# Performance work log

Hardware: AMD Instinct MI355X
Metric: run time of the kernel (lower is better)

Reference implementation:

```python
import jax, jax.numpy as jnp
import numpy as np

L, H, E, FF, B, S = 2, 8, 512, 2048, 8, 1024


def _layernorm(x, g, b, eps=1e-5):
    mu = jnp.mean(x, axis=-1, keepdims=True)
    var = jnp.mean(jnp.square(x - mu), axis=-1, keepdims=True)
    return (x - mu) * jax.lax.rsqrt(var + eps) * g + b


def setup_inputs() -> dict:
    key = jax.random.key(0)
    ks = jax.random.split(key, 16)
    sc = 1.0 / np.sqrt(E)
    d = {
        "x": jax.random.normal(ks[0], (B, S, E), jnp.float32),
        # per-layer, per-head disentangled projections: Linear(E,E) -> weight [out,in]
        "Wq": jax.random.normal(ks[1], (L, H, E, E), jnp.float32) * sc,
        "bq": jnp.zeros((L, H, E), jnp.float32),
        "Wk": jax.random.normal(ks[2], (L, H, E, E), jnp.float32) * sc,
        "bk": jnp.zeros((L, H, E), jnp.float32),
        "Wv": jax.random.normal(ks[3], (L, H, E, E), jnp.float32) * sc,
        "bv": jnp.zeros((L, H, E), jnp.float32),
        "Wo": jax.random.normal(ks[4], (L, H, E, E), jnp.float32) * sc,
        "bo": jnp.zeros((L, H, E), jnp.float32),
        "head_alphas": jax.random.uniform(ks[5], (H,), jnp.float32, 0.5, 1.5),
        "ln1_g": jnp.ones((L, E), jnp.float32),
        "ln1_b": jnp.zeros((L, E), jnp.float32),
        "W1": jax.random.normal(ks[6], (L, FF, E), jnp.float32) * sc,
        "b1": jnp.zeros((L, FF), jnp.float32),
        "W2": jax.random.normal(ks[7], (L, E, FF), jnp.float32) * (1.0 / np.sqrt(FF)),
        "b2": jnp.zeros((L, E), jnp.float32),
        "ln2_g": jnp.ones((L, E), jnp.float32),
        "ln2_b": jnp.zeros((L, E), jnp.float32),
    }
    return d


def reference(x, Wq, bq, Wk, bk, Wv, bv, Wo, bo, head_alphas,
              ln1_g, ln1_b, W1, b1, W2, b2, ln2_g, ln2_b):
    seq = x.shape[1]
    # causal additive mask, as generate_square_subsequent_mask
    causal = jnp.where(jnp.tril(jnp.ones((seq, seq), bool)), 0.0, -jnp.inf).astype(x.dtype)
    scale = jnp.sqrt(jnp.asarray(E, x.dtype))  # head_dim == embed_dim (disentangled)
    ha = head_alphas[None, :, None, None]
    for i in range(L):
        # disentangled per-head projections, batched over heads: [B,H,S,E]
        rq = jnp.einsum('bse,hoe->bhso', x, Wq[i]) + bq[i][None, :, None, :]
        rk = jnp.einsum('bse,hoe->bhso', x, Wk[i]) + bk[i][None, :, None, :]
        rv = jnp.einsum('bse,hoe->bhso', x, Wv[i]) + bv[i][None, :, None, :]
        scores = jnp.einsum('bhqd,bhkd->bhqk', rq, rk) / scale + causal
        attn = jax.nn.softmax(scores, axis=-1)
        ao = jnp.einsum('bhqk,bhkd->bhqd', attn, rv) * ha
        # per-head out_proj then sum over heads
        attn_out = jnp.einsum('bhsd,hod->bso', ao, Wo[i]) + jnp.sum(bo[i], axis=0)
        x = _layernorm(x + attn_out, ln1_g[i], ln1_b[i])
        h = jax.nn.relu(jnp.einsum('bse,fe->bsf', x, W1[i]) + b1[i])
        ff = jnp.einsum('bsf,ef->bse', h, W2[i]) + b2[i]
        x = _layernorm(x + ff, ln2_g[i], ln2_b[i])
    return x
```

## Files before the change

kernel.cpp:

```cpp
#include <hip/hip_runtime.h>
#include <hip/hip_bf16.h>
#include <stdint.h>

#define LL 2
#define HH 8
#define EE 512
#define FFD 2048
#define BB 8
#define SS 1024
#define CB 4
#define NCH (BB / CB)
#define PAIRS (CB * HH)

typedef unsigned short u16;
typedef __attribute__((ext_vector_type(8))) short bf16x8;
typedef __attribute__((ext_vector_type(4))) float f32x4;
typedef __attribute__((ext_vector_type(4))) int int4v;
typedef __attribute__((ext_vector_type(2))) int int2v;

__device__ __forceinline__ u16 f2bf(float f){
  union { float f; unsigned u; } c; c.f = f;
  unsigned r = (c.u + 0x7FFFu + ((c.u >> 16) & 1u)) >> 16;
  return (u16)r;
}

struct GP {
  const u16* A; const u16* B;
  const float* bias; const float* resid;
  void* out;
  long AsMHi, AsMLo, AsH;
  long BsNHi, BsNLo, BsH;
  long Abatch, Bbatch, Obatch, BiasB;
  long OsMHi, OsMLo, OsNHi, OsNLo;
  int M, N, K, causal, Kpart, cgrid;
  float scale;
};

__device__ __forceinline__ int xcd_swz(int bid, int nwg){
  if (nwg < 16) return bid;
  const int q = nwg >> 3, r = nwg & 7;
  const int xcd = bid & 7, loc = bid >> 3;
  return (xcd < r ? xcd * (q + 1) : r * (q + 1) + (xcd - r) * q) + loc;
}

template<int EP>
__global__ __launch_bounds__(256, 3) void k_gemm(GP p){
  const int tilesN = p.N >> 7;
  const int tilesM = p.M >> 7;
  const int bid = xcd_swz(blockIdx.x, gridDim.x);
  int mI, nI;
  if (p.cgrid){ nI = bid / tilesM; mI = bid % tilesM; }
  else        { mI = bid / tilesN; nI = bid % tilesN; }
  const int m0 = mI << 7;
  const int n0 = nI << 7;
  if (EP == 0 && p.causal && n0 > m0) return;
  const long bb = blockIdx.y;
  const u16* __restrict__ Ag = p.A + bb * p.Abatch;
  const u16* __restrict__ Bg = p.B + bb * p.Bbatch;

  __shared__ __align__(16) u16 As[128 * 64];
  __shared__ __align__(16) u16 Bs[128 * 64];
  char* AsB = (char*)As;
  char* BsB = (char*)Bs;

  const int t = threadIdx.x;
  const int lane = t & 63;
  const int wv = t >> 6;
  const int wr = (wv >> 1) << 6;
  const int wc = (wv & 1) << 6;

  long aoff[4], boff[4];
  #pragma unroll
  for (int j = 0; j < 4; ++j){
    const int r = ((wv << 2) + j) * 8 + (lane >> 3);
    const int kx = ((lane & 7) << 3) ^ ((r & 7) << 3);
    const int gm = m0 + r;
    aoff[j] = (long)(gm >> 10) * p.AsMHi + (long)(gm & 1023) * p.AsMLo + kx;
    const int gn = n0 + r;
    boff[j] = (long)(gn >> 9) * p.BsNHi + (long)(gn & 511) * p.BsNLo + kx;
  }

  int kBeg = 0;
  int Klim = p.K;
  if (EP == 2 && p.causal) { int kl = m0 + 128; Klim = kl < p.K ? kl : p.K; }
  if (EP == 5) { kBeg = (int)bb * p.Kpart; Klim = kBeg + p.Kpart; }

  f32x4 acc[4][4];
  #pragma unroll
  for (int a = 0; a < 4; ++a)
    #pragma unroll
    for (int b = 0; b < 4; ++b)
      acc[a][b] = (f32x4){0.f, 0.f, 0.f, 0.f};

  for (int k0 = kBeg; k0 < Klim; k0 += 64){
    const long ka = (long)(k0 >> 9) * p.AsH + (k0 & 511);
    const long kb = (long)(k0 >> 9) * p.BsH + (k0 & 511);
    __syncthreads();
    #pragma unroll
    for (int j = 0; j < 4; ++j){
      const int ldsOff = (((wv << 2) + j) << 9);
      __builtin_amdgcn_global_load_lds(
          (const __attribute__((address_space(1))) void*)(Ag + aoff[j] + ka),
          (__attribute__((address_space(3))) void*)(As + ldsOff), 16, 0, 0);
      __builtin_amdgcn_global_load_lds(
          (const __attribute__((address_space(1))) void*)(Bg + boff[j] + kb),
          (__attribute__((address_space(3))) void*)(Bs + ldsOff), 16, 0, 0);
    }
    __syncthreads();
    #pragma unroll
    for (int kk = 0; kk < 2; ++kk){
      bf16x8 af[4], bv[4];
      #pragma unroll
      for (int mi = 0; mi < 4; ++mi){
        int row = wr + (mi << 4) + (lane & 15);
        int bc = ((kk << 6) + ((lane >> 4) << 4)) ^ ((row & 7) << 4);
        af[mi] = *reinterpret_cast<const bf16x8*>(AsB + row * 128 + bc);
      }
      #pragma unroll
      for (int ni = 0; ni < 4; ++ni){
        int row = wc + (ni << 4) + (lane & 15);
        int bc = ((kk << 6) + ((lane >> 4) << 4)) ^ ((row & 7) << 4);
        bv[ni] = *reinterpret_cast<const bf16x8*>(BsB + row * 128 + bc);
      }
      #pragma unroll
      for (int mi = 0; mi < 4; ++mi)
        #pragma unroll
        for (int ni = 0; ni < 4; ++ni)
          acc[mi][ni] = __builtin_amdgcn_mfma_f32_16x16x32_bf16(af[mi], bv[ni], acc[mi][ni], 0, 0, 0);
    }
  }

  const int cm = (lane >> 4) << 2;
  const int cn = lane & 15;
  float biasv[4];
  if (EP == 1 || EP == 4){
    #pragma unroll
    for (int ni = 0; ni < 4; ++ni)
      biasv[ni] = p.bias[bb * p.BiasB + n0 + wc + (ni << 4) + cn];
  }
  #pragma unroll
  for (int mi = 0; mi < 4; ++mi){
    #pragma unroll
    for (int i = 0; i < 4; ++i){
      const int m = m0 + wr + (mi << 4) + cm + i;
      const long ob = bb * p.Obatch + (long)(m >> 10) * p.OsMHi + (long)(m & 1023) * p.OsMLo;
      #pragma unroll
      for (int ni = 0; ni < 4; ++ni){
        const int n = n0 + wc + (ni << 4) + cn;
        const long oa = ob + (long)(n >> 9) * p.OsNHi + (long)(n & 511) * p.OsNLo;
        float v = acc[mi][ni][i];
        if (EP == 0) ((u16*)p.out)[oa] = f2bf(v * p.scale);
        else if (EP == 1) ((u16*)p.out)[oa] = f2bf(v + biasv[ni]);
        else if (EP == 2) ((u16*)p.out)[oa] = f2bf(v);
        else if (EP == 5) ((float*)p.out)[oa] = v;
        else { float r = v + biasv[ni]; ((u16*)p.out)[oa] = f2bf(r > 0.f ? r : 0.f); }
      }
    }
  }
}

__global__ __launch_bounds__(128) void k_redln(const float* __restrict__ part,
                                               const float* __restrict__ bias,
                                               const float* __restrict__ resid,
                                               const float* __restrict__ g,
                                               const float* __restrict__ b,
                                               float* __restrict__ fdst,
                                               u16* __restrict__ bdst,
                                               long rowBase, long mn){
  const long lrow = blockIdx.x;
  const long row = rowBase + lrow;
  const int t = threadIdx.x;
  const int col = t << 2;
  const long poff = lrow * EE + col;
  const long off = row * EE + col;
  f32x4 s = *reinterpret_cast<const f32x4*>(part + poff);
  #pragma unroll
  for (int q = 1; q < 4; ++q){
    f32x4 v = *reinterpret_cast<const f32x4*>(part + q * mn + poff);
    s.x += v.x; s.y += v.y; s.z += v.z; s.w += v.w;
  }
  f32x4 bv = *reinterpret_cast<const f32x4*>(bias + col);
  f32x4 rv = *reinterpret_cast<const f32x4*>(resid + off);
  s.x += bv.x + rv.x; s.y += bv.y + rv.y; s.z += bv.z + rv.z; s.w += bv.w + rv.w;

  float ps = s.x + s.y + s.z + s.w;
  #pragma unroll
  for (int o = 32; o; o >>= 1) ps += __shfl_xor(ps, o);
  __shared__ float red[2], red2[2];
  if ((t & 63) == 0) red[t >> 6] = ps;
  __syncthreads();
  const float mean = (red[0] + red[1]) * (1.0f / EE);
  f32x4 d = { s.x - mean, s.y - mean, s.z - mean, s.w - mean };
  float pv = d.x * d.x + d.y * d.y + d.z * d.z + d.w * d.w;
  #pragma unroll
  for (int o = 32; o; o >>= 1) pv += __shfl_xor(pv, o);
  if ((t & 63) == 0) red2[t >> 6] = pv;
  __syncthreads();
  const float var = (red2[0] + red2[1]) * (1.0f / EE);
  const float rstd = rsqrtf(var + 1e-5f);
  f32x4 gv = *reinterpret_cast<const f32x4*>(g + col);
  f32x4 bb = *reinterpret_cast<const f32x4*>(b + col);
  f32x4 o4 = { d.x * rstd * gv.x + bb.x, d.y * rstd * gv.y + bb.y,
               d.z * rstd * gv.z + bb.z, d.w * rstd * gv.w + bb.w };
  *reinterpret_cast<f32x4*>(fdst + off) = o4;
  union { u16 us[4]; int2v v; } u;
  u.us[0] = f2bf(o4.x); u.us[1] = f2bf(o4.y);
  u.us[2] = f2bf(o4.z); u.us[3] = f2bf(o4.w);
  *reinterpret_cast<int2v*>(bdst + off) = u.v;
}

struct SetupP {
  const float *x, *bq, *bk, *bv, *bo;
  float *xf, *catb, *bos;
  u16 *xb;
};
#define SETUP_TA 524288u
#define SETUP_TC 25600u
__global__ __launch_bounds__(256) void k_setup(SetupP sp){
  const unsigned t = blockIdx.x * 256 + threadIdx.x;
  if (t < SETUP_TA){
    const int i = (int)t << 3;
    f32x4 a = *reinterpret_cast<const f32x4*>(sp.x + i);
    f32x4 b = *reinterpret_cast<const f32x4*>(sp.x + i + 4);
    *reinterpret_cast<f32x4*>(sp.xf + i) = a;
    *reinterpret_cast<f32x4*>(sp.xf + i + 4) = b;
    union { u16 us[8]; int4v v; } u;
    #pragma unroll
    for (int j = 0; j < 4; ++j){ u.us[j] = f2bf(a[j]); u.us[4 + j] = f2bf(b[j]); }
    *reinterpret_cast<int4v*>(sp.xb + i) = u.v;
  } else {
    const int j = (int)(t - SETUP_TA);
    if (j >= 2 * 12800) return;
    const int L = j / 12800;
    const int r = j - L * 12800;
    const int lw = L * HH * EE;
    float* catL = sp.catb + (size_t)L * 3 * HH * EE;
    if (r < 4096) catL[r] = sp.bq[lw + r];
    else if (r < 8192) catL[r] = sp.bk[lw + r - 4096];
    else if (r < 12288) catL[r] = sp.bv[lw + r - 8192];
    else {
      const int o = r - 12288;
      float s = 0.f;
      #pragma unroll
      for (int h = 0; h < HH; ++h) s += sp.bo[lw + h * EE + o];
      sp.bos[L * EE + o] = s;
    }
  }
}

struct WcvtP { const float *Wq, *Wk, *Wv, *Wo, *W1, *W2; u16* wdst; };
#define WCVT_T 1310720u
__global__ __launch_bounds__(256) void k_wcvt(WcvtP wp){
  const unsigned t = blockIdx.x * 256 + threadIdx.x;
  if (t >= WCVT_T) return;
  const size_t j = ((size_t)t) << 3;
  const size_t R = (size_t)2097152;
  const size_t F = (size_t)1048576;
  const float* src; size_t loc;
  if      (j < R)       { src = wp.Wq; loc = j; }
  else if (j < 2*R)     { src = wp.Wk; loc = j - R; }
  else if (j < 3*R)     { src = wp.Wv; loc = j - 2*R; }
  else if (j < 4*R)     { src = wp.Wo; loc = j - 3*R; }
  else if (j < 4*R + F) { src = wp.W1; loc = j - 4*R; }
  else                  { src = wp.W2; loc = j - 4*R - F; }
  f32x4 a = *reinterpret_cast<const f32x4*>(src + loc);
  f32x4 b = *reinterpret_cast<const f32x4*>(src + loc + 4);
  union { u16 us[8]; int4v v; } u;
  #pragma unroll
  for (int q = 0; q < 4; ++q){ u.us[q] = f2bf(a[q]); u.us[4 + q] = f2bf(b[q]); }
  *reinterpret_cast<int4v*>(wp.wdst + j) = u.v;
}

#define SM_BLOCKS (PAIRS * SS / 4)
__global__ __launch_bounds__(256) void k_smt(u16* __restrict__ sp,
                                             const float* __restrict__ alphas,
                                             const u16* __restrict__ v,
                                             u16* __restrict__ vt){
  if (blockIdx.x < SM_BLOCKS){
    const int wv = threadIdx.x >> 6;
    const long row = (long)blockIdx.x * 4 + wv;
    const int lane = threadIdx.x & 63;
    const int q = (int)(row & (SS - 1));
    const int h = (int)(row >> 10) & (HH - 1);
    const bool half2 = q >= 512;
    u16* rp = sp + row * SS;
    const int i0 = lane << 3;
    float vv[8], v2[8];
    float lm = -1e30f;
    {
      bf16x8 a = *reinterpret_cast<const bf16x8*>(rp + i0);
      #pragma unroll
      for (int j = 0; j < 8; ++j){
        union { unsigned u; float f; } c; c.u = ((unsigned)(u16)a[j]) << 16;
        vv[j] = (i0 + j <= q) ? c.f : -1e30f;
        lm = fmaxf(lm, vv[j]);
      }
    }
    if (half2){
      bf16x8 a = *reinterpret_cast<const bf16x8*>(rp + i0 + 512);
      #pragma unroll
      for (int j = 0; j < 8; ++j){
        union { unsigned u; float f; } c; c.u = ((unsigned)(u16)a[j]) << 16;
        v2[j] = (i0 + 512 + j <= q) ? c.f : -1e30f;
        lm = fmaxf(lm, v2[j]);
      }
    }
    #pragma unroll
    for (int o = 32; o; o >>= 1) lm = fmaxf(lm, __shfl_xor(lm, o));
    float ls = 0.f;
    #pragma unroll
    for (int j = 0; j < 8; ++j){
      float e = exp2f((vv[j] - lm) * 1.4426950408889634f);
      e = (i0 + j <= q) ? e : 0.f;
      vv[j] = e; ls += e;
    }
    if (half2){
      #pragma unroll
      for (int j = 0; j < 8; ++j){
        float e = exp2f((v2[j] - lm) * 1.4426950408889634f);
        e = (i0 + 512 + j <= q) ? e : 0.f;
        v2[j] = e; ls += e;
      }
    }
    #pragma unroll
    for (int o = 32; o; o >>= 1) ls += __shfl_xor(ls, o);
    const float inv = alphas[h] / ls;
    {
      union { u16 us[8]; bf16x8 v8; } o8;
      #pragma unroll
      for (int j = 0; j < 8; ++j) o8.us[j] = f2bf(vv[j] * inv);
      *reinterpret_cast<bf16x8*>(rp + i0) = o8.v8;
    }
    if (half2){
      union { u16 us[8]; bf16x8 v8; } o8;
      #pragma unroll
      for (int j = 0; j < 8; ++j) o8.us[j] = f2bf(v2[j] * inv);
      *reinterpret_cast<bf16x8*>(rp + i0 + 512) = o8.v8;
    }
  } else {
    const int bid2 = blockIdx.x - SM_BLOCKS;
    const long bh = bid2 >> 7;
    const int xy = bid2 & 127;
    const int ts = xy >> 3;
    const int td = xy & 7;
    const u16* src = v + bh * (long)(SS * EE) + (long)(ts * 64) * EE + td * 64;
    u16* dst = vt + bh * (long)(SS * EE) + (long)(td * 64) * SS + ts * 64;
    __shared__ __align__(16) u16 tl[64][80];
    const int t = threadIdx.x;
    #pragma unroll
    for (int it = 0; it < 2; ++it){
      int id = t + it * 256;
      int r = id >> 3, c = (id & 7) << 3;
      *reinterpret_cast<int4v*>(&tl[r][c]) =
          *reinterpret_cast<const int4v*>(src + (long)r * EE + c);
    }
    __syncthreads();
    #pragma unroll
    for (int it = 0; it < 2; ++it){
      int id = t + it * 256;
      int r = id >> 3, c = (id & 7) << 3;
      union { u16 us[8]; int4v v; } u;
      #pragma unroll
      for (int j = 0; j < 8; ++j) u.us[j] = tl[c + j][r];
      *reinterpret_cast<int4v*>(dst + (long)r * SS + c) = u.v;
    }
  }
}

static inline void gemm_launch(int EP, const GP& p, int batch, hipStream_t st){
  dim3 g((unsigned)((p.M >> 7) * (p.N >> 7)), (unsigned)batch);
  switch (EP){
    case 0: k_gemm<0><<<g, 256, 0, st>>>(p); break;
    case 1: k_gemm<1><<<g, 256, 0, st>>>(p); break;
    case 2: k_gemm<2><<<g, 256, 0, st>>>(p); break;
    case 4: k_gemm<4><<<g, 256, 0, st>>>(p); break;
    case 5: k_gemm<5><<<g, 256, 0, st>>>(p); break;
  }
}

extern "C" void kernel_launch(void* const* d_in, const int* in_sizes, int n_in,
                              void* d_out, int out_size, void* d_ws, size_t ws_size,
                              hipStream_t stream){
  const float* x    = (const float*)d_in[0];
  const float* Wq   = (const float*)d_in[1];
  const float* bq   = (const float*)d_in[2];
  const float* Wk   = (const float*)d_in[3];
  const float* bk   = (const float*)d_in[4];
  const float* Wv   = (const float*)d_in[5];
  const float* bv   = (const float*)d_in[6];
  const float* Wo   = (const float*)d_in[7];
  const float* bo   = (const float*)d_in[8];
  const float* alph = (const float*)d_in[9];
  const float* ln1g = (const float*)d_in[10];
  const float* ln1b = (const float*)d_in[11];
  const float* W1   = (const float*)d_in[12];
  const float* b1   = (const float*)d_in[13];
  const float* W2   = (const float*)d_in[14];
  const float* b2   = (const float*)d_in[15];
  const float* ln2g = (const float*)d_in[16];
  const float* ln2b = (const float*)d_in[17];
  float* out = (float*)d_out;

  const size_t nWh = (size_t)HH * EE * EE;
  const size_t nWf = (size_t)FFD * EE;
  const size_t nX  = (size_t)BB * SS * EE;
  const size_t nChQ = (size_t)CB * HH * SS * EE;
  const size_t nScC = (size_t)PAIRS * SS * SS;
  const size_t nXc  = (size_t)CB * SS * EE;

  char* w = (char*)d_ws;
  size_t off = 0;
  auto take = [&](size_t bytes) -> char* {
    char* p = w + off;
    off += (bytes + 255) & ~(size_t)255;
    return p;
  };

  u16* wqb = (u16*)take(2 * nWh);
  u16* wkb = (u16*)take(2 * nWh);
  u16* wvb = (u16*)take(2 * nWh);
  u16* wob = (u16*)take(2 * nWh);
  u16* w1b = (u16*)take(2 * nWf);
  u16* w2b = (u16*)take(2 * nWf);
  float* xf = (float*)take(4 * nX);
  u16* xb   = (u16*)take(2 * nX);
  u16* qc   = (u16*)take(2 * nChQ);
  u16* kc   = (u16*)take(2 * nChQ);
  u16* vc   = (u16*)take(2 * nChQ);
  u16* vtc  = (u16*)take(2 * nChQ);
  u16* sc   = (u16*)take(2 * nScC);
  float* bo_sum  = (float*)take(4 * 2 * EE);
  float* qkvbias = (float*)take(4 * 2 * 3 * HH * EE);
  float* partsC = (float*)qc;
  float* partsF = (float*)qc;
  u16* hid = sc;

  SetupP spp{ x, bq, bk, bv, bo, xf, qkvbias, bo_sum, xb };
  k_setup<<<dim3((SETUP_TA + SETUP_TC + 255) / 256), 256, 0, stream>>>(spp);

  for (int i = 0; i < LL; ++i){
    WcvtP wp{ Wq + (size_t)i * nWh, Wk + (size_t)i * nWh, Wv + (size_t)i * nWh,
              Wo + (size_t)i * nWh, W1 + (size_t)i * nWf, W2 + (size_t)i * nWf,
              wqb };
    k_wcvt<<<dim3(WCVT_T / 256), 256, 0, stream>>>(wp);

    for (int c = 0; c < NCH; ++c){
      const long rowBase = (long)c * CB * SS;

      GP p{};
      p.AsMHi = (long)1024 * EE; p.AsMLo = EE; p.AsH = 0;
      p.BsNHi = (long)EE * EE;   p.BsNLo = EE; p.BsH = 0;
      p.Abatch = 0; p.Bbatch = (long)nWh; p.Obatch = (long)nChQ;
      p.BiasB = (long)HH * EE;
      p.OsMHi = (long)HH * SS * EE; p.OsMLo = EE;
      p.OsNHi = (long)SS * EE; p.OsNLo = 1;
      p.M = CB * SS; p.N = HH * EE; p.K = EE;
      p.A = xb + (size_t)rowBase * EE;
      p.B = wqb; p.bias = qkvbias + (size_t)i * 3 * HH * EE;
      p.out = qc; p.scale = 1.f; p.causal = 0; p.resid = nullptr;
      p.Kpart = 0; p.cgrid = 1;
      gemm_launch(1, p, 3, stream);

      GP ps{};
      ps.A = qc; ps.B = kc; ps.out = sc;
      ps.AsMHi = 0; ps.AsMLo = EE; ps.AsH = 0;
      ps.BsNHi = (long)512 * EE; ps.BsNLo = EE; ps.BsH = 0;
      ps.Abatch = (long)SS * EE; ps.Bbatch = (long)SS * EE;
      ps.Obatch = (long)SS * SS; ps.BiasB = 0;
      ps.OsMHi = 0; ps.OsMLo = SS; ps.OsNHi = 512; ps.OsNLo = 1;
      ps.M = SS; ps.N = SS; ps.K = EE;
      ps.scale = 0.044194173824159216f; ps.causal = 1;
      ps.bias = nullptr; ps.resid = nullptr; ps.Kpart = 0; ps.cgrid = 0;
      gemm_launch(0, ps, PAIRS, stream);

      k_smt<<<dim3(SM_BLOCKS + 128 * PAIRS), 256, 0, stream>>>(sc, alph, vc, vtc);

      GP pv{};
      pv.A = sc; pv.B = vtc; pv.out = vc;
      pv.AsMHi = 0; pv.AsMLo = SS; pv.AsH = 512;
      pv.BsNHi = 0; pv.BsNLo = SS; pv.BsH = 512;
      pv.Abatch = (long)SS * SS; pv.Bbatch = (long)EE * SS;
      pv.Obatch = (long)SS * EE; pv.BiasB = 0;
      pv.OsMHi = 0; pv.OsMLo = EE; pv.OsNHi = 0; pv.OsNLo = 1;
      pv.M = SS; pv.N = EE; pv.K = SS; pv.causal = 1;
      pv.scale = 1.f; pv.bias = nullptr; pv.resid = nullptr;
      pv.Kpart = 0; pv.cgrid = 0;
      gemm_launch(2, pv, PAIRS, stream);

      GP pw{};
      pw.A = vc; pw.B = wob; pw.out = partsC;
      pw.AsMHi = (long)HH * SS * EE; pw.AsMLo = EE; pw.AsH = (long)SS * EE;
      pw.BsNHi = 0; pw.BsNLo = EE; pw.BsH = (long)EE * EE;
      pw.Abatch = pw.Bbatch = 0; pw.Obatch = (long)nXc; pw.BiasB = 0;
      pw.OsMHi = (long)1024 * EE; pw.OsMLo = EE; pw.OsNHi = 0; pw.OsNLo = 1;
      pw.M = CB * SS; pw.N = EE; pw.K = HH * EE; pw.Kpart = (HH * EE) / 4;
      pw.bias = nullptr; pw.resid = nullptr; pw.scale = 1.f; pw.causal = 0;
      pw.cgrid = 1;
      gemm_launch(5, pw, 4, stream);
      k_redln<<<dim3(CB * SS), 128, 0, stream>>>(partsC, bo_sum + (size_t)i * EE,
                                                 xf, ln1g + (size_t)i * EE,
                                                 ln1b + (size_t)i * EE, xf, xb,
                                                 rowBase, (long)nXc);
    }

    GP p1{};
    p1.A = xb; p1.B = w1b; p1.out = hid;
    p1.AsMHi = (long)1024 * EE; p1.AsMLo = EE; p1.AsH = 0;
    p1.BsNHi = (long)512 * EE; p1.BsNLo = EE; p1.BsH = 0;
    p1.Abatch = p1.Bbatch = p1.Obatch = 0; p1.BiasB = 0;
    p1.OsMHi = (long)1024 * FFD; p1.OsMLo = FFD; p1.OsNHi = 512; p1.OsNLo = 1;
    p1.M = BB * SS; p1.N = FFD; p1.K = EE;
    p1.bias = b1 + (size_t)i * FFD; p1.resid = nullptr; p1.scale = 1.f;
    p1.causal = 0; p1.Kpart = 0; p1.cgrid = 1;
    gemm_launch(4, p1, 1, stream);

    GP p2{};
    p2.A = hid; p2.B = w2b; p2.out = partsF;
    p2.AsMHi = (long)1024 * FFD; p2.AsMLo = FFD; p2.AsH = 512;
    p2.BsNHi = 0; p2.BsNLo = FFD; p2.BsH = 512;
    p2.Abatch = p2.Bbatch = 0; p2.Obatch = (long)nX; p2.BiasB = 0;
    p2.OsMHi = (long)1024 * EE; p2.OsMLo = EE; p2.OsNHi = 0; p2.OsNLo = 1;
    p2.M = BB * SS; p2.N = EE; p2.K = FFD; p2.Kpart = FFD / 4;
    p2.bias = nullptr; p2.resid = nullptr; p2.scale = 1.f; p2.causal = 0;
    p2.cgrid = 1;
    gemm_launch(5, p2, 4, stream);
    float* fdst = (i == LL - 1) ? out : xf;
    k_redln<<<dim3(BB * SS), 128, 0, stream>>>(partsF, b2 + (size_t)i * EE, xf,
                                               ln2g + (size_t)i * EE,
                                               ln2b + (size_t)i * EE, fdst, xb,
                                               0, (long)nX);
  }
}
```

Measured before the change: 1.131 ms.

## Double-buffer GEMM K-loop with BK=32 tiles and async LDS prefetch

The GEMM main loop now splits LDS into two 32-wide K buffers. It prefetches the next K slice via global_load_lds while MFMAs consume the current one, with manual vmcnt waits and barriers replacing the old load-then-compute pattern. The swizzle and fragment addressing are reworked for the 64-byte row stride, and launch bounds rise to 4 waves per SIMD. This aims to hide global-memory latency behind compute and raise occupancy. In exchange it halves the work per barrier, and the new swizzle may add LDS bank conflicts.

```diff
diff --git a/kernel.cpp b/kernel.cpp
--- a/kernel.cpp
+++ b/kernel.cpp
@@ -44,7 +44,7 @@
 }
 
 template<int EP>
-__global__ __launch_bounds__(256, 3) void k_gemm(GP p){
+__global__ __launch_bounds__(256, 4) void k_gemm(GP p){
   const int tilesN = p.N >> 7;
   const int tilesM = p.M >> 7;
   const int bid = xcd_swz(blockIdx.x, gridDim.x);
@@ -58,10 +58,8 @@
   const u16* __restrict__ Ag = p.A + bb * p.Abatch;
   const u16* __restrict__ Bg = p.B + bb * p.Bbatch;
 
-  __shared__ __align__(16) u16 As[128 * 64];
-  __shared__ __align__(16) u16 Bs[128 * 64];
-  char* AsB = (char*)As;
-  char* BsB = (char*)Bs;
+  __shared__ __align__(16) u16 As[2][128 * 32];
+  __shared__ __align__(16) u16 Bs[2][128 * 32];
 
   const int t = threadIdx.x;
   const int lane = t & 63;
@@ -69,16 +67,25 @@
   const int wr = (wv >> 1) << 6;
   const int wc = (wv & 1) << 6;
 
-  long aoff[4], boff[4];
-  #pragma unroll
-  for (int j = 0; j < 4; ++j){
-    const int r = ((wv << 2) + j) * 8 + (lane >> 3);
-    const int kx = ((lane & 7) << 3) ^ ((r & 7) << 3);
+  long aoff[2], boff[2];
+  #pragma unroll
+  for (int i = 0; i < 2; ++i){
+    const int r = (wv << 5) + (i << 4) + (lane >> 2);
+    const int kx = ((lane & 3) ^ ((lane >> 3) & 3)) << 3;
     const int gm = m0 + r;
-    aoff[j] = (long)(gm >> 10) * p.AsMHi + (long)(gm & 1023) * p.AsMLo + kx;
+    aoff[i] = (long)(gm >> 10) * p.AsMHi + (long)(gm & 1023) * p.AsMLo + kx;
     const int gn = n0 + r;
-    boff[j] = (long)(gn >> 9) * p.BsNHi + (long)(gn & 511) * p.BsNLo + kx;
-  }
+    boff[i] = (long)(gn >> 9) * p.BsNHi + (long)(gn & 511) * p.BsNLo + kx;
+  }
+
+  const int slotXor = (((lane >> 4) ^ ((lane >> 1) & 3)) << 4);
+  int afB[4], bvB[4];
+  #pragma unroll
+  for (int mi = 0; mi < 4; ++mi)
+    afB[mi] = (wr + (mi << 4) + (lane & 15)) * 64 + slotXor;
+  #pragma unroll
+  for (int ni = 0; ni < 4; ++ni)
+    bvB[ni] = (wc + (ni << 4) + (lane & 15)) * 64 + slotXor;
 
   int kBeg = 0;
   int Klim = p.K;
@@ -92,42 +99,49 @@
     for (int b = 0; b < 4; ++b)
       acc[a][b] = (f32x4){0.f, 0.f, 0.f, 0.f};
 
-  for (int k0 = kBeg; k0 < Klim; k0 += 64){
+  auto stage = [&](int buf, int k0){
     const long ka = (long)(k0 >> 9) * p.AsH + (k0 & 511);
     const long kb = (long)(k0 >> 9) * p.BsH + (k0 & 511);
-    __syncthreads();
-    #pragma unroll
-    for (int j = 0; j < 4; ++j){
-      const int ldsOff = (((wv << 2) + j) << 9);
+    #pragma unroll
+    for (int i = 0; i < 2; ++i){
+      const int ldsOff = (((wv << 1) + i) << 9);
       __builtin_amdgcn_global_load_lds(
-          (const __attribute__((address_space(1))) void*)(Ag + aoff[j] + ka),
-          (__attribute__((address_space(3))) void*)(As + ldsOff), 16, 0, 0);
+          (const __attribute__((address_space(1))) void*)(Ag + aoff[i] + ka),
+          (__attribute__((address_space(3))) void*)(&As[buf][ldsOff]), 16, 0, 0);
       __builtin_amdgcn_global_load_lds(
-          (const __attribute__((address_space(1))) void*)(Bg + boff[j] + kb),
-          (__attribute__((address_space(3))) void*)(Bs + ldsOff), 16, 0, 0);
-    }
-    __syncthreads();
-    #pragma unroll
-    for (int kk = 0; kk < 2; ++kk){
-      bf16x8 af[4], bv[4];
-      #pragma unroll
-      for (int mi = 0; mi < 4; ++mi){
-        int row = wr + (mi << 4) + (lane & 15);
-        int bc = ((kk << 6) + ((lane >> 4) << 4)) ^ ((row & 7) << 4);
-        af[mi] = *reinterpret_cast<const bf16x8*>(AsB + row * 128 + bc);
-      }
-      #pragma unroll
-      for (int ni = 0; ni < 4; ++ni){
-        int row = wc + (ni << 4) + (lane & 15);
-        int bc = ((kk << 6) + ((lane >> 4) << 4)) ^ ((row & 7) << 4);
-        bv[ni] = *reinterpret_cast<const bf16x8*>(BsB + row * 128 + bc);
-      }
-      #pragma unroll
-      for (int mi = 0; mi < 4; ++mi)
-        #pragma unroll
-        for (int ni = 0; ni < 4; ++ni)
-          acc[mi][ni] = __builtin_amdgcn_mfma_f32_16x16x32_bf16(af[mi], bv[ni], acc[mi][ni], 0, 0, 0);
-    }
+          (const __attribute__((address_space(1))) void*)(Bg + boff[i] + kb),
+          (__attribute__((address_space(3))) void*)(&Bs[buf][ldsOff]), 16, 0, 0);
+    }
+  };
+
+  stage(0, kBeg);
+  int cur = 0;
+  for (int k0 = kBeg; k0 < Klim; k0 += 32){
+    const int kn = k0 + 32;
+    if (kn < Klim){
+      stage(cur ^ 1, kn);
+      asm volatile("s_waitcnt vmcnt(4)" ::: "memory");
+    } else {
+      asm volatile("s_waitcnt vmcnt(0)" ::: "memory");
+    }
+    __builtin_amdgcn_s_barrier();
+    const char* AsB = (const char*)As[cur];
+    const char* BsB = (const char*)Bs[cur];
+    bf16x8 af[4], bv[4];
+    #pragma unroll
+    for (int mi = 0; mi < 4; ++mi)
+      af[mi] = *reinterpret_cast<const bf16x8*>(AsB + afB[mi]);
+    #pragma unroll
+    for (int ni = 0; ni < 4; ++ni)
+      bv[ni] = *reinterpret_cast<const bf16x8*>(BsB + bvB[ni]);
+    #pragma unroll
+    for (int mi = 0; mi < 4; ++mi)
+      #pragma unroll
+      for (int ni = 0; ni < 4; ++ni)
+        acc[mi][ni] = __builtin_amdgcn_mfma_f32_16x16x32_bf16(af[mi], bv[ni], acc[mi][ni], 0, 0, 0);
+    asm volatile("s_waitcnt lgkmcnt(0)" ::: "memory");
+    __builtin_amdgcn_s_barrier();
+    cur ^= 1;
   }
 
   const int cm = (lane >> 4) << 2;
```

New measurement: 1.196 ms. +5.7%, slower.
